# Kernel tuning notes

Measured on AMD Instinct MI355X. Metric: run time of the kernel, lower is better.

## Reference

```python
import jax, jax.numpy as jnp
import numpy as np

N = 8192       # nodes per graph
E = 262144     # edges per graph (avg degree 32)
H = 8          # attention heads
C = 128        # hidden dim per head (H*C = 1024 to match Linear(1024,128))
IN = 128       # input feature dim
NEG_SLOPE = 0.2


def _gat_conv(x, edge_index, W, att_src, att_dst, bias):
    """PyG GATConv (concat=True, add_self_loops=True, shared lin for src/dst)."""
    n = x.shape[0]
    loop = jnp.arange(n, dtype=edge_index.dtype)
    src = jnp.concatenate([edge_index[0], loop])  # [E+N]
    dst = jnp.concatenate([edge_index[1], loop])
    h = (x @ W).reshape(n, H, C)                         # [N,H,C]
    a_src = jnp.sum(h * att_src, axis=-1)                # [N,H]
    a_dst = jnp.sum(h * att_dst, axis=-1)                # [N,H]
    e = jax.nn.leaky_relu(a_src[src] + a_dst[dst], NEG_SLOPE)   # [E+N,H]
    m = jax.ops.segment_max(e, dst, num_segments=n)      # per-dst max for stability
    ex = jnp.exp(e - m[dst])
    den = jax.ops.segment_sum(ex, dst, num_segments=n)
    alpha = ex / den[dst]                                # [E+N,H] neighborhood softmax
    out = jax.ops.segment_sum(h[src] * alpha[:, :, None], dst, num_segments=n)
    return out.reshape(n, H * C) + bias                  # [N, H*C]


def setup_inputs() -> dict:
    key = jax.random.key(0)
    ks = jax.random.split(key, 12)
    s = 0.05  # keep activations in a sane range
    return {
        "x1": jax.random.normal(ks[0], (N, IN), jnp.float32),
        "edge_index1": jax.random.randint(ks[1], (2, E), 0, N, dtype=jnp.int64),
        "W1": jax.random.normal(ks[2], (IN, H * C), jnp.float32) * s,
        "att_src1": jax.random.normal(ks[3], (H, C), jnp.float32) * s,
        "att_dst1": jax.random.normal(ks[4], (H, C), jnp.float32) * s,
        "b1": jnp.zeros((H * C,), jnp.float32),
        "x2": jax.random.normal(ks[5], (N, IN), jnp.float32),
        "edge_index2": jax.random.randint(ks[6], (2, E), 0, N, dtype=jnp.int64),
        "W2": jax.random.normal(ks[7], (IN, H * C), jnp.float32) * s,
        "att_src2": jax.random.normal(ks[8], (H, C), jnp.float32) * s,
        "att_dst2": jax.random.normal(ks[9], (H, C), jnp.float32) * s,
        "b2": jnp.zeros((H * C,), jnp.float32),
        "Wl": jax.random.normal(ks[10], (H * C, 128), jnp.float32) * s,
        "bl": jnp.zeros((128,), jnp.float32),
    }


def reference(x1, edge_index1, W1, att_src1, att_dst1, b1,
              x2, edge_index2, W2, att_src2, att_dst2, b2, Wl, bl):
    emb1 = _gat_conv(x1, edge_index1, W1, att_src1, att_dst1, b1)  # [N1,1024]
    emb2 = _gat_conv(x2, edge_index2, W2, att_src2, att_dst2, b2)  # [N2,1024]
    scores = emb1 @ emb2.T                                          # [N1,N2]
    w1 = jax.nn.softmax(scores, axis=1)
    w2 = jax.nn.softmax(scores, axis=0)
    cross1 = (w2 @ emb2) @ Wl + bl      # [N1,128]
    cross2 = (w1.T @ emb1) @ Wl + bl    # [N2,128]
    return (jnp.mean(cross1, axis=0), jnp.mean(cross2, axis=0))
```

## Files before the change

### kernel.cpp

```cpp
#include <hip/hip_runtime.h>


#define NN 8192
#define EE 262144
#define NEG 0.2f

#define BKT 128
#define RNG (NN / BKT)
#define CAP 2560
#define CHK (EE / 128)

#define U_CNT   0
#define U_GACC  (U_CNT + 4*BKT)
#define U_ZEND  (U_GACC + 2048)
#define U_U     (U_ZEND)
#define U_MEMB  (U_U + 2*2048)
#define U_ASRC  (U_MEMB + 2048)
#define U_ADST  (U_ASRC + 2*NN*8)
#define U_PR    (U_ADST + 2*NN*8)
#define U_BIND  (U_PR + 2*NN*16)
#define U_BINS  (U_BIND + 2*BKT*CAP)
#define ZERO_BYTES ((size_t)U_ZEND * 4)

__global__ __launch_bounds__(512) void k_bin(
    const int* __restrict__ ei1, const int* __restrict__ ei2,
    const float* __restrict__ W1, const float* __restrict__ as1,
    const float* __restrict__ ad1,
    const float* __restrict__ W2, const float* __restrict__ as2,
    const float* __restrict__ ad2,
    int* __restrict__ cnt, int* __restrict__ binD, int* __restrict__ binS,
    float* __restrict__ u) {
  int g = blockIdx.y;
  int t = threadIdx.x;
  if (blockIdx.x >= 128) {
    int sd = blockIdx.x - 128;
    const float* Wg = g ? W2 : W1;
    const float* att = g ? (sd ? ad2 : as2) : (sd ? ad1 : as1);
    float* uo = u + g * 2048 + sd * 1024;
    for (int o = t; o < 1024; o += 512) {
      int head = o >> 7, k = o & 127;
      const float4* wr = (const float4*)(Wg + (size_t)k * 1024 + head * 128);
      const float4* ar = (const float4*)(att + head * 128);
      float s = 0.f;
#pragma unroll 8
      for (int c = 0; c < 32; ++c) {
        float4 w4 = wr[c], a4 = ar[c];
        s += w4.x * a4.x + w4.y * a4.y + w4.z * a4.z + w4.w * a4.w;
      }
      uo[o] = s;
    }
    return;
  }
  const int* ei = g ? ei2 : ei1;
  __shared__ int hD[BKT], hS[BKT], bD[BKT], bS[BKT], cD[BKT], cS[BKT];
  for (int i = t; i < BKT; i += 512) { hD[i] = 0; hS[i] = 0; cD[i] = 0; cS[i] = 0; }
  __syncthreads();
  int e0 = blockIdx.x * CHK;
  for (int i = t; i < CHK; i += 512) {
    int s = ei[e0 + i], d = ei[EE + e0 + i];
    atomicAdd(&hD[d >> 6], 1);
    atomicAdd(&hS[s >> 6], 1);
  }
  __syncthreads();
  for (int i = t; i < BKT; i += 512) {
    bD[i] = atomicAdd(cnt + (2 * g + 0) * BKT + i, hD[i]);
    bS[i] = atomicAdd(cnt + (2 * g + 1) * BKT + i, hS[i]);
  }
  __syncthreads();
  int* bdg = binD + (size_t)g * BKT * CAP;
  int* bsg = binS + (size_t)g * BKT * CAP;
  for (int i = t; i < CHK; i += 512) {
    int s = ei[e0 + i], d = ei[EE + e0 + i];
    int kb = d >> 6;
    int p = bD[kb] + atomicAdd(&cD[kb], 1);
    bdg[kb * CAP + p] = (s << 6) | (d & 63);
    kb = s >> 6;
    p = bS[kb] + atomicAdd(&cS[kb], 1);
    bsg[kb * CAP + p] = (d << 6) | (s & 63);
  }
}

__global__ __launch_bounds__(512) void k_a(
    const float* __restrict__ x1, const float* __restrict__ x2,
    const float* __restrict__ u,
    float* __restrict__ asrc, float* __restrict__ adst) {
  int gph = blockIdx.y, cb = blockIdx.x;
  __shared__ float xs[64][129];
  __shared__ float us[16][128];
  int t = threadIdx.x;
  const float* ug = u + gph * 2048;
  for (int i = t; i < 2048; i += 512) us[i >> 7][i & 127] = ug[i];
  const float* x = gph ? x2 : x1;
  const int n0 = cb * 64;
  const float4* xb4 = (const float4*)(x + (size_t)n0 * 128);
  for (int i = t; i < 64 * 32; i += 512) {
    float4 v = xb4[i];
    int r = i >> 5, c = (i & 31) * 4;
    xs[r][c] = v.x; xs[r][c + 1] = v.y; xs[r][c + 2] = v.z; xs[r][c + 3] = v.w;
  }
  __syncthreads();
  int nl = t & 63;
  int j0 = (t >> 6) * 2;
  float a0 = 0.f, a1 = 0.f;
#pragma unroll 4
  for (int k = 0; k < 128; ++k) {
    float xv = xs[nl][k];
    a0 += xv * us[j0 + 0][k];
    a1 += xv * us[j0 + 1][k];
  }
  int n = n0 + nl;
  float* outp = (j0 < 8) ? (asrc + gph * (NN * 8) + n * 8 + j0)
                         : (adst + gph * (NN * 8) + n * 8 + (j0 - 8));
  outp[0] = a0; outp[1] = a1;
}

__global__ __launch_bounds__(512) void k_den(
    const int* __restrict__ cnt, const int* __restrict__ binD,
    const float* __restrict__ asrc, const float* __restrict__ adst,
    float* __restrict__ pr) {
  int gph = blockIdx.y, b = blockIdx.x;
  int lo = b * RNG;
  const float* as = asrc + gph * (NN * 8);
  const float* ad = adst + gph * (NN * 8);
  float2* prg = (float2*)pr + (size_t)gph * (NN * 8);
  __shared__ float den[RNG * 8];
  __shared__ float ads[RNG * 8];
  int t = threadIdx.x;
  for (int i = t; i < RNG * 8; i += 512) {
    float avv = ad[lo * 8 + i];
    float v = as[lo * 8 + i] + avv;
    v = v > 0.f ? v : NEG * v;
    ads[i] = avv;
    den[i] = __expf(v);
  }
  __syncthreads();
  int n = cnt[(2 * gph + 0) * BKT + b];
  const int* recs = binD + (size_t)gph * BKT * CAP + b * CAP;
  int rid = t >> 3, h = t & 7;
  for (int base = 0; base < n; base += 256) {
    int rv[4]; bool ok[4]; float sv[4];
#pragma unroll
    for (int uu = 0; uu < 4; ++uu) {
      int i = base + uu * 64 + rid;
      ok[uu] = i < n;
      rv[uu] = ok[uu] ? recs[i] : 0;
    }
#pragma unroll
    for (int uu = 0; uu < 4; ++uu)
      sv[uu] = ok[uu] ? as[(rv[uu] >> 6) * 8 + h] : 0.f;
#pragma unroll
    for (int uu = 0; uu < 4; ++uu) {
      if (ok[uu]) {
        int dl = rv[uu] & 63;
        float v = sv[uu] + ads[dl * 8 + h];
        v = v > 0.f ? v : NEG * v;
        atomicAdd(&den[dl * 8 + h], __expf(v));
      }
    }
  }
  __syncthreads();
  for (int i = t; i < RNG * 8; i += 512)
    prg[lo * 8 + i] = make_float2(ads[i], 1.0f / den[i]);
}

__global__ __launch_bounds__(512) void k_waccG(
    const int* __restrict__ cnt, const int* __restrict__ binS,
    const float* __restrict__ asrc, const float* __restrict__ pr,
    const float* __restrict__ x1, const float* __restrict__ x2,
    float* __restrict__ gacc) {
  int gph = blockIdx.y, b = blockIdx.x;
  int lo = b * RNG;
  const float* as = asrc + gph * (NN * 8);
  const float2* prg = (const float2*)pr + (size_t)gph * (NN * 8);
  __shared__ float wv[RNG * 8];
  __shared__ float asx[RNG * 8];
  int t = threadIdx.x;
  for (int i = t; i < RNG * 8; i += 512) {
    float sva = as[lo * 8 + i];
    float2 f2 = prg[lo * 8 + i];
    float v = sva + f2.x;
    v = v > 0.f ? v : NEG * v;
    asx[i] = sva;
    wv[i] = __expf(v) * f2.y;
  }
  __syncthreads();
  int n = cnt[(2 * gph + 1) * BKT + b];
  const int* recs = binS + (size_t)gph * BKT * CAP + b * CAP;
  int rid = t >> 3, h = t & 7;
  for (int base = 0; base < n; base += 256) {
    int rv[4]; bool ok[4]; float2 pv[4];
#pragma unroll
    for (int uu = 0; uu < 4; ++uu) {
      int i = base + uu * 64 + rid;
      ok[uu] = i < n;
      rv[uu] = ok[uu] ? recs[i] : 0;
    }
#pragma unroll
    for (int uu = 0; uu < 4; ++uu)
      pv[uu] = ok[uu] ? prg[(size_t)(rv[uu] >> 6) * 8 + h] : make_float2(0.f, 0.f);
#pragma unroll
    for (int uu = 0; uu < 4; ++uu) {
      if (ok[uu]) {
        int sl = rv[uu] & 63;
        float v = asx[sl * 8 + h] + pv[uu].x;
        v = v > 0.f ? v : NEG * v;
        atomicAdd(&wv[sl * 8 + h], __expf(v) * pv[uu].y);
      }
    }
  }
  __syncthreads();
  const float* x = gph ? x2 : x1;
  float* gg = gacc + gph * 1024;
  int k = t & 127;
  int h0 = (t >> 7) * 2;
  int n0 = b * RNG;
  float a0 = 0.f, a1 = 0.f;
#pragma unroll 4
  for (int nl = 0; nl < RNG; ++nl) {
    float xv = x[(size_t)(n0 + nl) * 128 + k];
    a0 += xv * wv[nl * 8 + h0];
    a1 += xv * wv[nl * 8 + h0 + 1];
  }
  atomicAdd(gg + (h0 + 0) * 128 + k, a0);
  atomicAdd(gg + (h0 + 1) * 128 + k, a1);
}

__global__ __launch_bounds__(512) void k_memb(
    const float* __restrict__ gacc,
    const float* __restrict__ W1, const float* __restrict__ b1,
    const float* __restrict__ W2, const float* __restrict__ b2,
    float* __restrict__ memb) {
  int g = blockIdx.y;
  int e0 = blockIdx.x * 64;
  const float* W = g ? W2 : W1;
  const float* bb = g ? b2 : b1;
  const float* gr = gacc + g * 1024 + (e0 >> 7) * 128;
  __shared__ float pm[8][64];
  int t = threadIdx.x;
  int el = t & 63, kc = t >> 6;
  int e = e0 + el;
  float s = 0.f;
#pragma unroll
  for (int k = kc * 16; k < kc * 16 + 16; ++k)
    s += gr[k] * W[(size_t)k * 1024 + e];
  pm[kc][el] = s;
  __syncthreads();
  if (t < 64) {
    float acc = pm[0][el];
#pragma unroll
    for (int q = 1; q < 8; ++q) acc += pm[q][el];
    memb[g * 1024 + e] = acc * (1.0f / (float)NN) + bb[e];
  }
}

__global__ __launch_bounds__(256) void k_out(
    const float* __restrict__ memb, const float* __restrict__ Wl,
    const float* __restrict__ bl, float* __restrict__ out) {
  int t = threadIdx.x;
  int j = t & 127;
  int k0 = blockIdx.x * 32;
  const float* m = (t < 128) ? (memb + 1024) : memb;
  float s = 0.f;
#pragma unroll
  for (int k = k0; k < k0 + 32; ++k) s += m[k] * Wl[(size_t)k * 128 + j];
  if (blockIdx.x == 0) s += bl[j];
  atomicAdd(out + t, s);
}

extern "C" void kernel_launch(void* const* d_in, const int* in_sizes, int n_in,
                              void* d_out, int out_size, void* d_ws, size_t ws_size,
                              hipStream_t stream) {
  const float* x1  = (const float*)d_in[0];
  const int*   ei1 = (const int*)d_in[1];
  const float* W1  = (const float*)d_in[2];
  const float* as1 = (const float*)d_in[3];
  const float* ad1 = (const float*)d_in[4];
  const float* b1  = (const float*)d_in[5];
  const float* x2  = (const float*)d_in[6];
  const int*   ei2 = (const int*)d_in[7];
  const float* W2  = (const float*)d_in[8];
  const float* as2 = (const float*)d_in[9];
  const float* ad2 = (const float*)d_in[10];
  const float* b2  = (const float*)d_in[11];
  const float* Wl  = (const float*)d_in[12];
  const float* bl  = (const float*)d_in[13];
  float* out = (float*)d_out;

  int*   cnt  = (int*)d_ws + U_CNT;
  float* gacc = (float*)d_ws + U_GACC;
  float* u    = (float*)d_ws + U_U;
  float* memb = (float*)d_ws + U_MEMB;
  float* asrc = (float*)d_ws + U_ASRC;
  float* adst = (float*)d_ws + U_ADST;
  float* pr   = (float*)d_ws + U_PR;
  int*   binD = (int*)d_ws + U_BIND;
  int*   binS = (int*)d_ws + U_BINS;

  hipMemsetAsync(d_ws, 0, ZERO_BYTES, stream);
  hipMemsetAsync(d_out, 0, (size_t)out_size * 4, stream);

  k_bin<<<dim3(130, 2), 512, 0, stream>>>(ei1, ei2, W1, as1, ad1,
                                          W2, as2, ad2, cnt, binD, binS, u);
  k_a<<<dim3(128, 2), 512, 0, stream>>>(x1, x2, u, asrc, adst);
  k_den<<<dim3(BKT, 2), 512, 0, stream>>>(cnt, binD, asrc, adst, pr);
  k_waccG<<<dim3(BKT, 2), 512, 0, stream>>>(cnt, binS, asrc, pr, x1, x2, gacc);
  k_memb<<<dim3(16, 2), 512, 0, stream>>>(gacc, W1, b1, W2, b2, memb);
  k_out<<<32, 256, 0, stream>>>(memb, Wl, bl, out);
}
```

Measured before the change: 179.3 us.

## Cache edges in registers during binning, deepen gather unroll, drop output memset

k_bin now loads each edge once into registers and reuses the local atomic slot from the histogram pass, which removes the second global read of the edge list and the second round of shared atomics. k_den and k_waccG process 8 records per thread per iteration instead of 4, putting more independent gathers in flight at the cost of more registers. k_out is rewritten so each block writes its outputs directly after a shared-memory reduction, which removes the output memset and the global atomics. The edge-register path assumes CHK equals 4*512 exactly.

```diff
diff --git a/kernel.cpp b/kernel.cpp
--- a/kernel.cpp
+++ b/kernel.cpp
@@ -52,14 +52,21 @@
     return;
   }
   const int* ei = g ? ei2 : ei1;
-  __shared__ int hD[BKT], hS[BKT], bD[BKT], bS[BKT], cD[BKT], cS[BKT];
-  for (int i = t; i < BKT; i += 512) { hD[i] = 0; hS[i] = 0; cD[i] = 0; cS[i] = 0; }
+  __shared__ int hD[BKT], hS[BKT], bD[BKT], bS[BKT];
+  for (int i = t; i < BKT; i += 512) { hD[i] = 0; hS[i] = 0; }
   __syncthreads();
   int e0 = blockIdx.x * CHK;
-  for (int i = t; i < CHK; i += 512) {
-    int s = ei[e0 + i], d = ei[EE + e0 + i];
-    atomicAdd(&hD[d >> 6], 1);
-    atomicAdd(&hS[s >> 6], 1);
+  int sE[4], dE[4], lD[4], lS[4];
+#pragma unroll
+  for (int uu = 0; uu < 4; ++uu) {
+    int i = e0 + uu * 512 + t;
+    sE[uu] = ei[i];
+    dE[uu] = ei[EE + i];
+  }
+#pragma unroll
+  for (int uu = 0; uu < 4; ++uu) {
+    lD[uu] = atomicAdd(&hD[dE[uu] >> 6], 1);
+    lS[uu] = atomicAdd(&hS[sE[uu] >> 6], 1);
   }
   __syncthreads();
   for (int i = t; i < BKT; i += 512) {
@@ -69,14 +76,12 @@
   __syncthreads();
   int* bdg = binD + (size_t)g * BKT * CAP;
   int* bsg = binS + (size_t)g * BKT * CAP;
-  for (int i = t; i < CHK; i += 512) {
-    int s = ei[e0 + i], d = ei[EE + e0 + i];
-    int kb = d >> 6;
-    int p = bD[kb] + atomicAdd(&cD[kb], 1);
-    bdg[kb * CAP + p] = (s << 6) | (d & 63);
-    kb = s >> 6;
-    p = bS[kb] + atomicAdd(&cS[kb], 1);
-    bsg[kb * CAP + p] = (d << 6) | (s & 63);
+#pragma unroll
+  for (int uu = 0; uu < 4; ++uu) {
+    int kb = dE[uu] >> 6;
+    bdg[kb * CAP + bD[kb] + lD[uu]] = (sE[uu] << 6) | (dE[uu] & 63);
+    kb = sE[uu] >> 6;
+    bsg[kb * CAP + bS[kb] + lS[uu]] = (dE[uu] << 6) | (sE[uu] & 63);
   }
 }
 
@@ -137,19 +142,19 @@
   int n = cnt[(2 * gph + 0) * BKT + b];
   const int* recs = binD + (size_t)gph * BKT * CAP + b * CAP;
   int rid = t >> 3, h = t & 7;
-  for (int base = 0; base < n; base += 256) {
-    int rv[4]; bool ok[4]; float sv[4];
-#pragma unroll
-    for (int uu = 0; uu < 4; ++uu) {
+  for (int base = 0; base < n; base += 512) {
+    int rv[8]; bool ok[8]; float sv[8];
+#pragma unroll
+    for (int uu = 0; uu < 8; ++uu) {
       int i = base + uu * 64 + rid;
       ok[uu] = i < n;
       rv[uu] = ok[uu] ? recs[i] : 0;
     }
 #pragma unroll
-    for (int uu = 0; uu < 4; ++uu)
+    for (int uu = 0; uu < 8; ++uu)
       sv[uu] = ok[uu] ? as[(rv[uu] >> 6) * 8 + h] : 0.f;
 #pragma unroll
-    for (int uu = 0; uu < 4; ++uu) {
+    for (int uu = 0; uu < 8; ++uu) {
       if (ok[uu]) {
         int dl = rv[uu] & 63;
         float v = sv[uu] + ads[dl * 8 + h];
@@ -187,19 +192,19 @@
   int n = cnt[(2 * gph + 1) * BKT + b];
   const int* recs = binS + (size_t)gph * BKT * CAP + b * CAP;
   int rid = t >> 3, h = t & 7;
-  for (int base = 0; base < n; base += 256) {
-    int rv[4]; bool ok[4]; float2 pv[4];
-#pragma unroll
-    for (int uu = 0; uu < 4; ++uu) {
+  for (int base = 0; base < n; base += 512) {
+    int rv[8]; bool ok[8]; float2 pv[8];
+#pragma unroll
+    for (int uu = 0; uu < 8; ++uu) {
       int i = base + uu * 64 + rid;
       ok[uu] = i < n;
       rv[uu] = ok[uu] ? recs[i] : 0;
     }
 #pragma unroll
-    for (int uu = 0; uu < 4; ++uu)
+    for (int uu = 0; uu < 8; ++uu)
       pv[uu] = ok[uu] ? prg[(size_t)(rv[uu] >> 6) * 8 + h] : make_float2(0.f, 0.f);
 #pragma unroll
-    for (int uu = 0; uu < 4; ++uu) {
+    for (int uu = 0; uu < 8; ++uu) {
       if (ok[uu]) {
         int sl = rv[uu] & 63;
         float v = asx[sl * 8 + h] + pv[uu].x;
@@ -253,18 +258,31 @@
   }
 }
 
-__global__ __launch_bounds__(256) void k_out(
+__global__ __launch_bounds__(512) void k_out(
     const float* __restrict__ memb, const float* __restrict__ Wl,
     const float* __restrict__ bl, float* __restrict__ out) {
-  int t = threadIdx.x;
-  int j = t & 127;
-  int k0 = blockIdx.x * 32;
-  const float* m = (t < 128) ? (memb + 1024) : memb;
+  __shared__ float ml[1024];
+  __shared__ float po[16][32];
+  int b = blockIdx.x;
+  int t = threadIdx.x;
+  const float* m = (b < 4) ? (memb + 1024) : memb;
+  for (int i = t; i < 1024; i += 512) ml[i] = m[i];
+  __syncthreads();
+  int ol = t & 31, kc = t >> 5;
+  int o = b * 32 + ol;
+  int j = o & 127;
   float s = 0.f;
-#pragma unroll
-  for (int k = k0; k < k0 + 32; ++k) s += m[k] * Wl[(size_t)k * 128 + j];
-  if (blockIdx.x == 0) s += bl[j];
-  atomicAdd(out + t, s);
+#pragma unroll 8
+  for (int k = kc * 64; k < kc * 64 + 64; ++k)
+    s += ml[k] * Wl[(size_t)k * 128 + j];
+  po[kc][ol] = s;
+  __syncthreads();
+  if (t < 32) {
+    float acc = po[0][t];
+#pragma unroll
+    for (int q = 1; q < 16; ++q) acc += po[q][t];
+    out[b * 32 + t] = acc + bl[(b * 32 + t) & 127];
+  }
 }
 
 extern "C" void kernel_launch(void* const* d_in, const int* in_sizes, int n_in,
@@ -297,7 +315,6 @@
   int*   binS = (int*)d_ws + U_BINS;
 
   hipMemsetAsync(d_ws, 0, ZERO_BYTES, stream);
-  hipMemsetAsync(d_out, 0, (size_t)out_size * 4, stream);
 
   k_bin<<<dim3(130, 2), 512, 0, stream>>>(ei1, ei2, W1, as1, ad1,
                                           W2, as2, ad2, cnt, binD, binS, u);
@@ -305,5 +322,5 @@
   k_den<<<dim3(BKT, 2), 512, 0, stream>>>(cnt, binD, asrc, adst, pr);
   k_waccG<<<dim3(BKT, 2), 512, 0, stream>>>(cnt, binS, asrc, pr, x1, x2, gacc);
   k_memb<<<dim3(16, 2), 512, 0, stream>>>(gacc, W1, b1, W2, b2, memb);
-  k_out<<<32, 256, 0, stream>>>(memb, Wl, bl, out);
-}
+  k_out<<<8, 512, 0, stream>>>(memb, Wl, bl, out);
+}
```

Result: slower. 183.4 us (+2.3%).
